# Kernel optimization log

Hardware: AMD Instinct MI355X
Metric: run time of the kernel (lower is better)

The kernel has to match this reference:

```python
import jax, jax.numpy as jnp
import numpy as np

B, T, H, I, O, R = 64, 1024, 1024, 8, 8, 4
NOISE_STD, ALPHA = 0.05, 0.2


def setup_inputs() -> dict:
    key = jax.random.key(0)
    ks = jax.random.split(key, 6)
    return {
        "x": jax.random.normal(ks[0], (B, T, I), jnp.float32),
        "noise": jax.random.normal(ks[1], (B, T, H), jnp.float32),
        "wi": jax.random.normal(ks[2], (I, H), jnp.float32),
        "si": jnp.ones((I,), jnp.float32),
        "m": jax.random.normal(ks[3], (H, R), jnp.float32),
        "n": jax.random.normal(ks[4], (H, R), jnp.float32),
        "b": jnp.zeros((H,), jnp.float32),
        "wo": jax.random.normal(ks[5], (H, O), jnp.float32) / H,
        "so": jnp.ones((O,), jnp.float32),
        "h0": jnp.zeros((H,), jnp.float32),
    }


def reference(x, noise, wi, si, m, n, b, wo, so, h0):
    hidden = h0.shape[0]
    batch = x.shape[0]
    wi_full = wi * si[:, None]          # (I, H): (wi.T * si).T
    wo_full = wo * so                   # (H, O)
    h_init = jnp.broadcast_to(h0, (batch, hidden))
    r_init = jnp.tanh(h_init)           # non_linearity(initial_states)
    # precompute input drive for all steps: (B,T,H) -> scan over time-major
    u = jnp.einsum('bti,ih->tbh', x, wi_full)
    noise_t = jnp.transpose(noise, (1, 0, 2))  # (T,B,H)

    def step(carry, inp):
        h, r = carry
        u_i, nz_i = inp
        rec = (r @ n) @ m.T / hidden                    # low-rank recurrence
        h = h + NOISE_STD * nz_i + ALPHA * (-h + rec + u_i)
        r = jnp.tanh(h + b)
        out = h @ wo_full                               # identity output nonlin
        return (h, r), out

    _, outs = jax.lax.scan(step, (h_init, r_init), (u, noise_t))
    return jnp.transpose(outs, (1, 0, 2))  # (B,T,O)
```

## Files before the change

### kernel.cpp

```cpp
#include <hip/hip_runtime.h>

#define BB 64
#define TT 1024
#define HH 1024
#define II 8
#define OO 8
#define RRK 4
#define NOISE_STD 0.05f
#define ALPHA 0.2f

typedef float v4f __attribute__((ext_vector_type(4)));

#define C2E 2.885390081777927f

template<int CTRL, int RM>
__device__ __forceinline__ float dpp_add(float acc, float src) {
    int s = __builtin_amdgcn_update_dpp(0, __float_as_int(src), CTRL, RM, 0xF, true);
    return acc + __int_as_float(s);
}

__device__ __forceinline__ float wave_sum(float x) {
    x = dpp_add<0xB1, 0xF>(x, x);
    x = dpp_add<0x4E, 0xF>(x, x);
    x = dpp_add<0x141, 0xF>(x, x);
    x = dpp_add<0x140, 0xF>(x, x);
    x = dpp_add<0x142, 0xA>(x, x);
    x = dpp_add<0x143, 0xC>(x, x);
    return x;
}

__device__ __forceinline__ float tanh_from_l2x(float l2x) {
    float e = __builtin_amdgcn_exp2f(l2x);
    float r = __builtin_amdgcn_rcpf(e + 1.0f);
    return fmaf(-2.0f, r, 1.0f);
}

__device__ __forceinline__ void block_sync_lds() {
    asm volatile("s_waitcnt lgkmcnt(0)\n\ts_barrier" ::: "memory");
}


__global__ __launch_bounds__(256)
void pre_d_kernel(const float* __restrict__ x, const float* __restrict__ noise,
                  const float* __restrict__ wi, const float* __restrict__ si,
                  const float* __restrict__ wo, const float* __restrict__ so,
                  float* __restrict__ d, float* __restrict__ sbase) {
    __shared__ __align__(16) float red[2][8][4][8];

    const int tid  = threadIdx.x;
    const int wave = tid >> 6;
    const int lane = tid & 63;
    const int e0   = tid << 2;

    v4f wia4[II];
    #pragma unroll
    for (int i = 0; i < II; ++i)
        wia4[i] = (ALPHA * si[i]) * *(const v4f*)(wi + (size_t)i * HH + e0);

    float woa[4][OO];
    #pragma unroll
    for (int e = 0; e < 4; ++e) {
        const float4 a4 = *(const float4*)(wo + (e0 + e) * OO);
        const float4 b4 = *(const float4*)(wo + (e0 + e) * OO + 4);
        woa[e][0] = a4.x * so[0]; woa[e][1] = a4.y * so[1];
        woa[e][2] = a4.z * so[2]; woa[e][3] = a4.w * so[3];
        woa[e][4] = b4.x * so[4]; woa[e][5] = b4.y * so[5];
        woa[e][6] = b4.z * so[6]; woa[e][7] = b4.w * so[7];
    }

    const int row0 = blockIdx.x * 32;
    float4 nz[8], nzn[8];
    #pragma unroll
    for (int j = 0; j < 8; ++j)
        nz[j] = *(const float4*)(noise + (size_t)(row0 + j) * HH + e0);

    #pragma unroll
    for (int ph = 0; ph < 4; ++ph) {
        const int cur   = ph & 1;
        const int rbase = row0 + ph * 8;

        if (ph < 3) {
            #pragma unroll
            for (int j = 0; j < 8; ++j)
                nzn[j] = *(const float4*)(noise + (size_t)(rbase + 8 + j) * HH + e0);
        }

        #pragma unroll
        for (int j = 0; j < 8; ++j) {
            const int row = rbase + j;
            const float4 xr0 = *(const float4*)(x + (size_t)row * II);
            const float4 xr1 = *(const float4*)(x + (size_t)row * II + 4);
            v4f u = xr0.x * wia4[0];
            u += xr0.y * wia4[1];  u += xr0.z * wia4[2];
            u += xr0.w * wia4[3];  u += xr1.x * wia4[4];
            u += xr1.y * wia4[5];  u += xr1.z * wia4[6];
            u += xr1.w * wia4[7];
            v4f d4 = u;
            d4.x = fmaf(NOISE_STD, nz[j].x, d4.x);
            d4.y = fmaf(NOISE_STD, nz[j].y, d4.y);
            d4.z = fmaf(NOISE_STD, nz[j].z, d4.z);
            d4.w = fmaf(NOISE_STD, nz[j].w, d4.w);
            *(v4f*)(d + (size_t)row * HH + e0) = d4;

            float op[OO];
            #pragma unroll
            for (int o = 0; o < OO; ++o)
                op[o] = fmaf(d4.x, woa[0][o], fmaf(d4.y, woa[1][o],
                        fmaf(d4.z, woa[2][o], d4.w * woa[3][o])));
            #pragma unroll
            for (int o = 0; o < OO; ++o) op[o] = wave_sum(op[o]);
            if (lane == 63) {
                *(float4*)&red[cur][j][wave][0] = make_float4(op[0], op[1], op[2], op[3]);
                *(float4*)&red[cur][j][wave][4] = make_float4(op[4], op[5], op[6], op[7]);
            }
        }
        block_sync_lds();
        if (tid < 64) {
            const int j = tid >> 3, o = tid & 7;
            sbase[(rbase + j) * OO + o] = (red[cur][j][0][o] + red[cur][j][1][o]) +
                                          (red[cur][j][2][o] + red[cur][j][3][o]);
        }
        #pragma unroll
        for (int j = 0; j < 8; ++j) nz[j] = nzn[j];
    }
}

__global__ __launch_bounds__(512, 1)
void rnn_pair(const float* __restrict__ d, const float* __restrict__ sbase,
              const float* __restrict__ mM, const float* __restrict__ nM,
              const float* __restrict__ bv, const float* __restrict__ wo,
              const float* __restrict__ so, const float* __restrict__ h0,
              float* __restrict__ out) {
    __shared__ __align__(16) float lds_v[2][TT * RRK];
    __shared__ __align__(16) float red[2][4][4][RRK];
    __shared__ __align__(16) float redc[8][40];
    __shared__ __align__(16) float amy[40];
    __shared__ __align__(16) float chs[2][32][OO];

    const int tid  = threadIdx.x;
    const int wave = tid >> 6;
    const int lane = tid & 63;
    const int sg   = wave >> 2;
    const int rw   = wave & 3;
    const int tl   = tid & 255;
    const int b    = blockIdx.x * 2 + sg;
    const int hb   = rw * 256 + lane * 4;
    const int oc   = tid & 7;

    {
        const int e2 = tid << 1;
        const float cs = ALPHA / (float)HH;
        const v4f m0 = cs * *(const v4f*)(mM + (size_t)e2 * RRK);
        const v4f m1 = cs * *(const v4f*)(mM + (size_t)(e2 + 1) * RRK);
        float wp0[OO], wp1[OO];
        {
            const float4 a4 = *(const float4*)(wo + (size_t)e2 * OO);
            const float4 b4 = *(const float4*)(wo + (size_t)e2 * OO + 4);
            wp0[0] = a4.x * so[0]; wp0[1] = a4.y * so[1];
            wp0[2] = a4.z * so[2]; wp0[3] = a4.w * so[3];
            wp0[4] = b4.x * so[4]; wp0[5] = b4.y * so[5];
            wp0[6] = b4.z * so[6]; wp0[7] = b4.w * so[7];
            const float4 c4 = *(const float4*)(wo + (size_t)(e2 + 1) * OO);
            const float4 d4 = *(const float4*)(wo + (size_t)(e2 + 1) * OO + 4);
            wp1[0] = c4.x * so[0]; wp1[1] = c4.y * so[1];
            wp1[2] = c4.z * so[2]; wp1[3] = c4.w * so[3];
            wp1[4] = d4.x * so[4]; wp1[5] = d4.y * so[5];
            wp1[6] = d4.z * so[6]; wp1[7] = d4.w * so[7];
        }
        const float ha = h0[e2], hc = h0[e2 + 1];
        #pragma unroll
        for (int kg = 0; kg < 10; ++kg) {
            float p[4];
            #pragma unroll
            for (int u = 0; u < 4; ++u) {
                const int k = kg * 4 + u;
                float s;
                if (k < 32) {
                    const int q = k >> 3, o = k & 7;
                    s = fmaf(m0[q], wp0[o], m1[q] * wp1[o]);
                } else {
                    const int o = k - 32;
                    s = fmaf(ha, wp0[o], hc * wp1[o]);
                }
                p[u] = wave_sum(s);
            }
            if (lane == 63)
                *(float4*)&redc[wave][kg * 4] = make_float4(p[0], p[1], p[2], p[3]);
        }
    }
    block_sync_lds();
    if (tid < 40)
        amy[tid] = ((redc[0][tid] + redc[1][tid]) + (redc[2][tid] + redc[3][tid])) +
                   ((redc[4][tid] + redc[5][tid]) + (redc[6][tid] + redc[7][tid]));

    v4f nrv[4], mac[RRK], h, r, tb2;
    {
        const float cs = ALPHA / (float)HH;
        v4f mrow[4];
        #pragma unroll
        for (int e = 0; e < 4; ++e) {
            nrv[e]  = *(const v4f*)(nM + (size_t)(hb + e) * RRK);
            mrow[e] = cs * *(const v4f*)(mM + (size_t)(hb + e) * RRK);
        }
        #pragma unroll
        for (int q = 0; q < RRK; ++q)
            mac[q] = (v4f){mrow[0][q], mrow[1][q], mrow[2][q], mrow[3][q]};
        h   = *(const v4f*)(h0 + hb);
        tb2 = C2E * *(const v4f*)(bv + hb);
        const v4f tg = C2E * h;
        r.x = tanh_from_l2x(tg.x); r.y = tanh_from_l2x(tg.y);
        r.z = tanh_from_l2x(tg.z); r.w = tanh_from_l2x(tg.w);
    }

    const float* dp = d + (size_t)b * (TT * HH) + hb;
    v4f dbuf[4];
    #pragma unroll
    for (int j = 0; j < 4; ++j)
        dbuf[j] = *(const v4f*)(dp + (size_t)j * HH);

    for (int t0 = 0; t0 < TT; t0 += 4) {
        #pragma unroll
        for (int j = 0; j < 4; ++j) {
            const int t = t0 + j;

            v4f vp = r.x * nrv[0];
            vp += r.y * nrv[1];
            vp += r.z * nrv[2];
            vp += r.w * nrv[3];
            const float s0 = wave_sum(vp.x);
            const float s1 = wave_sum(vp.y);
            const float s2 = wave_sum(vp.z);
            const float s3 = wave_sum(vp.w);
            if (lane == 63)
                *(float4*)&red[sg][j][rw][0] = make_float4(s0, s1, s2, s3);

            block_sync_lds();

            const v4f p0 = *(const v4f*)&red[sg][j][0][0];
            const v4f p1 = *(const v4f*)&red[sg][j][1][0];
            const v4f p2 = *(const v4f*)&red[sg][j][2][0];
            const v4f p3 = *(const v4f*)&red[sg][j][3][0];
            const v4f vs = (p0 + p1) + (p2 + p3);
            if (tl == 0) *(v4f*)&lds_v[sg][t * RRK] = vs;

            v4f acc = dbuf[j];
            acc += vs.x * mac[0];
            acc += vs.y * mac[1];
            acc += vs.z * mac[2];
            acc += vs.w * mac[3];
            h = (1.0f - ALPHA) * h + acc;

            dbuf[j] = *(const v4f*)(dp + (size_t)((t + 4) & (TT - 1)) * HH);

            const v4f tg = C2E * h + tb2;
            r.x = tanh_from_l2x(tg.x); r.y = tanh_from_l2x(tg.y);
            r.z = tanh_from_l2x(tg.z); r.w = tanh_from_l2x(tg.w);
        }
    }

    __syncthreads();

    float Amr[RRK];
    #pragma unroll
    for (int q = 0; q < RRK; ++q) Amr[q] = amy[q * 8 + oc];

    const int c  = tl >> 3;
    const int tc = c * 32;
    float a32;
    {
        float a = 1.0f - ALPHA;
        a = a * a; a = a * a; a = a * a; a = a * a; a = a * a;
        a32 = a;
    }
    const float* sb = sbase + (size_t)b * (TT * OO);

    auto step_s = [&](int t) -> float {
        const v4f vv = *(const v4f*)&lds_v[sg][t * RRK];
        float s = sb[t * OO + oc];
        s = fmaf(vv.x, Amr[0], s); s = fmaf(vv.y, Amr[1], s);
        s = fmaf(vv.z, Amr[2], s); s = fmaf(vv.w, Amr[3], s);
        return s;
    };

    float L = 0.0f;
    #pragma unroll 4
    for (int jt = 0; jt < 32; ++jt)
        L = fmaf(1.0f - ALPHA, L, step_s(tc + jt));
    chs[sg][c][oc] = L;
    block_sync_lds();
    if (tl < OO) {
        float Y = amy[32 + tl];
        #pragma unroll 4
        for (int c2 = 0; c2 < 32; ++c2) {
            const float Lc = chs[sg][c2][tl];
            chs[sg][c2][tl] = Y;
            Y = fmaf(a32, Y, Lc);
        }
    }
    block_sync_lds();
    float yv = chs[sg][c][oc];
    float* ob = out + (size_t)b * (TT * OO);
    #pragma unroll 4
    for (int jt = 0; jt < 32; ++jt) {
        const int t = tc + jt;
        yv = fmaf(1.0f - ALPHA, yv, step_s(t));
        ob[t * OO + oc] = yv;
    }
}


__global__ __launch_bounds__(256)
void prew_fb(const float* __restrict__ noise, const float* __restrict__ wo,
             const float* __restrict__ so, float* __restrict__ W) {
    __shared__ __align__(16) float red[2][8][4][8];

    const int tid  = threadIdx.x;
    const int wave = tid >> 6;
    const int lane = tid & 63;
    const int e0   = tid << 2;

    float woa[4][OO];
    {
        float so8[OO];
        #pragma unroll
        for (int o = 0; o < OO; ++o) so8[o] = so[o] * NOISE_STD;
        #pragma unroll
        for (int e = 0; e < 4; ++e) {
            const float4 a4 = *(const float4*)(wo + (e0 + e) * OO);
            const float4 b4 = *(const float4*)(wo + (e0 + e) * OO + 4);
            woa[e][0] = a4.x * so8[0]; woa[e][1] = a4.y * so8[1];
            woa[e][2] = a4.z * so8[2]; woa[e][3] = a4.w * so8[3];
            woa[e][4] = b4.x * so8[4]; woa[e][5] = b4.y * so8[5];
            woa[e][6] = b4.z * so8[6]; woa[e][7] = b4.w * so8[7];
        }
    }

    const int row0 = blockIdx.x * 32;
    float4 nz[8], nzn[8];
    #pragma unroll
    for (int j = 0; j < 8; ++j)
        nz[j] = *(const float4*)(noise + (size_t)(row0 + j) * HH + e0);

    #pragma unroll
    for (int ph = 0; ph < 4; ++ph) {
        const int cur   = ph & 1;
        const int rbase = row0 + ph * 8;
        if (ph < 3) {
            #pragma unroll
            for (int j = 0; j < 8; ++j)
                nzn[j] = *(const float4*)(noise + (size_t)(rbase + 8 + j) * HH + e0);
        }
        #pragma unroll
        for (int j = 0; j < 8; ++j) {
            float op[OO];
            #pragma unroll
            for (int o = 0; o < OO; ++o)
                op[o] = fmaf(nz[j].x, woa[0][o], fmaf(nz[j].y, woa[1][o],
                        fmaf(nz[j].z, woa[2][o], nz[j].w * woa[3][o])));
            #pragma unroll
            for (int o = 0; o < OO; ++o) op[o] = wave_sum(op[o]);
            if (lane == 63) {
                *(float4*)&red[cur][j][wave][0] = make_float4(op[0], op[1], op[2], op[3]);
                *(float4*)&red[cur][j][wave][4] = make_float4(op[4], op[5], op[6], op[7]);
            }
        }
        block_sync_lds();
        if (tid < 64) {
            const int j = tid >> 3, o = tid & 7;
            W[(rbase + j) * OO + o] = (red[cur][j][0][o] + red[cur][j][1][o]) +
                                      (red[cur][j][2][o] + red[cur][j][3][o]);
        }
        #pragma unroll
        for (int j = 0; j < 8; ++j) nz[j] = nzn[j];
    }
}

__global__ __launch_bounds__(256, 1)
void rnn_fb(const float* __restrict__ x, const float* __restrict__ noise,
            const float* __restrict__ wi, const float* __restrict__ si,
            const float* __restrict__ mM, const float* __restrict__ nM,
            const float* __restrict__ bv, const float* __restrict__ wo,
            const float* __restrict__ so, const float* __restrict__ h0,
            const float* __restrict__ W, float* __restrict__ out) {
    __shared__ __align__(16) float lds_x[(TT + 1) * II];
    __shared__ __align__(16) float lds_W[TT * OO];
    __shared__ __align__(16) float lds_out[TT * OO];
    __shared__ __align__(16) float red[4][4][4];
    __shared__ __align__(16) float redc[4][104];
    __shared__ float ambx[104];

    const int tid  = threadIdx.x;
    const int b    = blockIdx.x;
    const int wave = tid >> 6;
    const int lane = tid & 63;
    const int e0   = tid << 2;
    const int oc   = tid & 7;

    {
        const float4* sx = (const float4*)(x + (size_t)b * (TT * II));
        const float4* sw = (const float4*)(W + (size_t)b * (TT * OO));
        float4* dx = (float4*)lds_x;
        float4* dw = (float4*)lds_W;
        #pragma unroll
        for (int k = 0; k < 8; ++k) {
            dx[k * 256 + tid] = sx[k * 256 + tid];
            dw[k * 256 + tid] = sw[k * 256 + tid];
        }
        if (tid < 2) dx[2048 + tid] = sx[2046 + tid];
    }

    float wia[II][4];
    v4f   wiac[II];
    #pragma unroll
    for (int i = 0; i < II; ++i) {
        const float s  = ALPHA * si[i];
        const float4 w = *(const float4*)(wi + i * HH + e0);
        wia[i][0] = w.x * s; wia[i][1] = w.y * s; wia[i][2] = w.z * s; wia[i][3] = w.w * s;
        wiac[i] = (v4f){wia[i][0], wia[i][1], wia[i][2], wia[i][3]};
    }
    float ma[4][RRK];
    v4f   nrv[4];
    v4f   mac[RRK];
    #pragma unroll
    for (int e = 0; e < 4; ++e) {
        const float4 m4 = *(const float4*)(mM + (e0 + e) * RRK);
        const float4 n4 = *(const float4*)(nM + (e0 + e) * RRK);
        const float cs = ALPHA / (float)HH;
        ma[e][0] = m4.x * cs; ma[e][1] = m4.y * cs; ma[e][2] = m4.z * cs; ma[e][3] = m4.w * cs;
        nrv[e] = (v4f){n4.x, n4.y, n4.z, n4.w};
    }
    #pragma unroll
    for (int q = 0; q < RRK; ++q)
        mac[q] = (v4f){ma[0][q], ma[1][q], ma[2][q], ma[3][q]};

    float woa[4][OO];
    {
        #pragma unroll
        for (int e = 0; e < 4; ++e) {
            const float4 a4 = *(const float4*)(wo + (e0 + e) * OO);
            const float4 b4 = *(const float4*)(wo + (e0 + e) * OO + 4);
            woa[e][0] = a4.x * so[0]; woa[e][1] = a4.y * so[1];
            woa[e][2] = a4.z * so[2]; woa[e][3] = a4.w * so[3];
            woa[e][4] = b4.x * so[4]; woa[e][5] = b4.y * so[5];
            woa[e][6] = b4.z * so[6]; woa[e][7] = b4.w * so[7];
        }
    }
    v4f tb2e, h, rr;
    {
        const v4f b4 = *(const v4f*)(bv + e0);
        tb2e = C2E * b4;
        h = *(const v4f*)(h0 + e0);
        v4f targ = C2E * h;
        rr.x = tanh_from_l2x(targ.x); rr.y = tanh_from_l2x(targ.y);
        rr.z = tanh_from_l2x(targ.z); rr.w = tanh_from_l2x(targ.w);
    }

    #pragma unroll
    for (int kg = 0; kg < 26; ++kg) {
        float p[4];
        #pragma unroll
        for (int u = 0; u < 4; ++u) {
            const int k = kg * 4 + u;
            float s;
            if (k < 32) {
                const int q = k >> 3, o = k & 7;
                s = fmaf(ma[0][q], woa[0][o], fmaf(ma[1][q], woa[1][o],
                    fmaf(ma[2][q], woa[2][o], ma[3][q] * woa[3][o])));
            } else if (k < 96) {
                const int i = (k - 32) >> 3, o = k & 7;
                s = fmaf(wia[i][0], woa[0][o], fmaf(wia[i][1], woa[1][o],
                    fmaf(wia[i][2], woa[2][o], wia[i][3] * woa[3][o])));
            } else {
                const int o = k - 96;
                s = fmaf(h.x, woa[0][o], fmaf(h.y, woa[1][o],
                    fmaf(h.z, woa[2][o], h.w * woa[3][o])));
            }
            p[u] = wave_sum(s);
        }
        if (lane == 63)
            *(float4*)&redc[wave][kg * 4] = make_float4(p[0], p[1], p[2], p[3]);
    }
    block_sync_lds();
    if (tid < 104)
        ambx[tid] = (redc[0][tid] + redc[1][tid]) + (redc[2][tid] + redc[3][tid]);
    __syncthreads();

    float Amr[RRK], Bxr[II], y;
    #pragma unroll
    for (int q = 0; q < RRK; ++q) Amr[q] = ambx[q * 8 + oc];
    #pragma unroll
    for (int i = 0; i < II; ++i) Bxr[i] = ambx[32 + i * 8 + oc];
    y = ambx[96 + oc];

    const float* nzp = noise + (size_t)b * (TT * HH) + e0;
    v4f nzb[4];
    #pragma unroll
    for (int j = 0; j < 4; ++j) nzb[j] = *(const v4f*)(nzp + j * HH);

    v4f xqc0 = *(const v4f*)&lds_x[0];
    v4f xqc1 = *(const v4f*)&lds_x[4];
    float wqc = lds_W[oc];

    for (int t0 = 0; t0 < TT; t0 += 4) {
        #pragma unroll
        for (int j = 0; j < 4; ++j) {
            const int t = t0 + j;
            const int tn = t + 1;
            const v4f xqn0 = *(const v4f*)&lds_x[tn * II];
            const v4f xqn1 = *(const v4f*)&lds_x[tn * II + 4];
            const float wqn = lds_W[(tn & (TT - 1)) * OO + oc];

            v4f vpv = rr.x * nrv[0];
            vpv += rr.y * nrv[1];
            vpv += rr.z * nrv[2];
            vpv += rr.w * nrv[3];
            float vp0 = wave_sum(vpv.x);
            float vp1 = wave_sum(vpv.y);
            float vp2 = wave_sum(vpv.z);
            float vp3 = wave_sum(vpv.w);
            if (lane == 63)
                *(float4*)&red[j][wave][0] = make_float4(vp0, vp1, vp2, vp3);

            float ybase = fmaf(xqc0.x, Bxr[0], wqc);
            ybase = fmaf(xqc0.y, Bxr[1], ybase);
            ybase = fmaf(xqc0.z, Bxr[2], ybase);
            ybase = fmaf(xqc0.w, Bxr[3], ybase);
            ybase = fmaf(xqc1.x, Bxr[4], ybase);
            ybase = fmaf(xqc1.y, Bxr[5], ybase);
            ybase = fmaf(xqc1.z, Bxr[6], ybase);
            ybase = fmaf(xqc1.w, Bxr[7], ybase);

            v4f auv = xqc0.x * wiac[0];
            auv += xqc0.y * wiac[1];
            auv += xqc0.z * wiac[2];
            auv += xqc0.w * wiac[3];
            auv += xqc1.x * wiac[4];
            auv += xqc1.y * wiac[5];
            auv += xqc1.z * wiac[6];
            auv += xqc1.w * wiac[7];

            block_sync_lds();

            const v4f s0 = *(const v4f*)&red[j][0][0];
            const v4f s1 = *(const v4f*)&red[j][1][0];
            const v4f s2 = *(const v4f*)&red[j][2][0];
            const v4f s3 = *(const v4f*)&red[j][3][0];
            const v4f vs = (s0 + s1) + (s2 + s3);

            v4f acc = auv;
            acc += vs.x * mac[0];
            acc += vs.y * mac[1];
            acc += vs.z * mac[2];
            acc += vs.w * mac[3];
            h = (1.0f - ALPHA) * h + acc;
            h += NOISE_STD * nzb[j];

            {
                float t4 = fmaf(vs.x, Amr[0], ybase);
                t4 = fmaf(vs.y, Amr[1], t4);
                t4 = fmaf(vs.z, Amr[2], t4);
                t4 = fmaf(vs.w, Amr[3], t4);
                y = fmaf(1.0f - ALPHA, y, t4);
                if (tid < OO) lds_out[t * OO + tid] = y;
            }

            nzb[j] = *(const v4f*)(nzp + ((t + 4) & (TT - 1)) * HH);

            {
                v4f targ = C2E * h + tb2e;
                rr.x = tanh_from_l2x(targ.x);
                rr.y = tanh_from_l2x(targ.y);
                rr.z = tanh_from_l2x(targ.z);
                rr.w = tanh_from_l2x(targ.w);
            }
            xqc0 = xqn0; xqc1 = xqn1; wqc = wqn;
        }
    }

    __syncthreads();
    {
        float4* dst = (float4*)(out + (size_t)b * (TT * OO));
        const float4* srcv = (const float4*)lds_out;
        #pragma unroll
        for (int k = 0; k < 8; ++k)
            dst[k * 256 + tid] = srcv[k * 256 + tid];
    }
}

extern "C" void kernel_launch(void* const* d_in, const int* in_sizes, int n_in,
                              void* d_out, int out_size, void* d_ws, size_t ws_size,
                              hipStream_t stream) {
    const float* x     = (const float*)d_in[0];
    const float* noise = (const float*)d_in[1];
    const float* wi    = (const float*)d_in[2];
    const float* si    = (const float*)d_in[3];
    const float* mM    = (const float*)d_in[4];
    const float* nM    = (const float*)d_in[5];
    const float* bv    = (const float*)d_in[6];
    const float* wo    = (const float*)d_in[7];
    const float* so    = (const float*)d_in[8];
    const float* h0    = (const float*)d_in[9];
    float* out = (float*)d_out;

    const size_t needD = (size_t)BB * TT * HH * sizeof(float);
    const size_t needS = (size_t)BB * TT * OO * sizeof(float);

    if (ws_size >= needD + needS) {
        float* dbuf = (float*)d_ws;
        float* sb   = dbuf + (size_t)BB * TT * HH;
        pre_d_kernel<<<dim3(2048), dim3(256), 0, stream>>>(
            x, noise, wi, si, wo, so, dbuf, sb);
        rnn_pair<<<dim3(BB / 2), dim3(512), 0, stream>>>(
            dbuf, sb, mM, nM, bv, wo, so, h0, out);
    } else {
        float* W = (float*)d_ws;
        prew_fb<<<dim3(2048), dim3(256), 0, stream>>>(noise, wo, so, W);
        rnn_fb<<<dim3(BB), dim3(256), 0, stream>>>(
            x, noise, wi, si, mM, nM, bv, wo, so, h0, W, out);
    }
}
```

Baseline: 909.6 us.

## Interleave two batch recurrences per 256-thread block instead of two 256-thread subgroups

The recurrent kernel now uses 256 threads per block. Each thread carries the hidden state for both batch elements of the pair, so the two independent recurrences are interleaved inside one instruction stream and share one barrier per step. Before, each batch had its own 4-wave subgroup in a 512-thread block. The aim is to hide the latency of the serial reduction and tanh chain with independent work and to halve the waves that take part in each barrier. The cost is more registers and longer per-wave work per step, and the output scan now uses 64-step chunks.

```diff
diff --git a/kernel.cpp b/kernel.cpp
--- a/kernel.cpp
+++ b/kernel.cpp
@@ -33,6 +33,13 @@
     float e = __builtin_amdgcn_exp2f(l2x);
     float r = __builtin_amdgcn_rcpf(e + 1.0f);
     return fmaf(-2.0f, r, 1.0f);
+}
+
+__device__ __forceinline__ v4f tanh4(v4f tg) {
+    v4f r;
+    r.x = tanh_from_l2x(tg.x); r.y = tanh_from_l2x(tg.y);
+    r.z = tanh_from_l2x(tg.z); r.w = tanh_from_l2x(tg.w);
+    return r;
 }
 
 __device__ __forceinline__ void block_sync_lds() {
@@ -125,78 +132,28 @@
     }
 }
 
-__global__ __launch_bounds__(512, 1)
-void rnn_pair(const float* __restrict__ d, const float* __restrict__ sbase,
-              const float* __restrict__ mM, const float* __restrict__ nM,
-              const float* __restrict__ bv, const float* __restrict__ wo,
-              const float* __restrict__ so, const float* __restrict__ h0,
-              float* __restrict__ out) {
+__global__ __launch_bounds__(256, 1)
+void rnn_pair2(const float* __restrict__ d, const float* __restrict__ sbase,
+               const float* __restrict__ mM, const float* __restrict__ nM,
+               const float* __restrict__ bv, const float* __restrict__ wo,
+               const float* __restrict__ so, const float* __restrict__ h0,
+               float* __restrict__ out) {
     __shared__ __align__(16) float lds_v[2][TT * RRK];
     __shared__ __align__(16) float red[2][4][4][RRK];
-    __shared__ __align__(16) float redc[8][40];
+    __shared__ __align__(16) float redc[4][40];
     __shared__ __align__(16) float amy[40];
-    __shared__ __align__(16) float chs[2][32][OO];
+    __shared__ __align__(16) float chs[2][16][OO];
 
     const int tid  = threadIdx.x;
     const int wave = tid >> 6;
     const int lane = tid & 63;
-    const int sg   = wave >> 2;
-    const int rw   = wave & 3;
-    const int tl   = tid & 255;
-    const int b    = blockIdx.x * 2 + sg;
-    const int hb   = rw * 256 + lane * 4;
+    const int hb   = tid << 2;
     const int oc   = tid & 7;
-
-    {
-        const int e2 = tid << 1;
+    const int bA   = blockIdx.x * 2;
+
+    v4f nrv[4], mrow[4], mac[RRK], tb2;
+    {
         const float cs = ALPHA / (float)HH;
-        const v4f m0 = cs * *(const v4f*)(mM + (size_t)e2 * RRK);
-        const v4f m1 = cs * *(const v4f*)(mM + (size_t)(e2 + 1) * RRK);
-        float wp0[OO], wp1[OO];
-        {
-            const float4 a4 = *(const float4*)(wo + (size_t)e2 * OO);
-            const float4 b4 = *(const float4*)(wo + (size_t)e2 * OO + 4);
-            wp0[0] = a4.x * so[0]; wp0[1] = a4.y * so[1];
-            wp0[2] = a4.z * so[2]; wp0[3] = a4.w * so[3];
-            wp0[4] = b4.x * so[4]; wp0[5] = b4.y * so[5];
-            wp0[6] = b4.z * so[6]; wp0[7] = b4.w * so[7];
-            const float4 c4 = *(const float4*)(wo + (size_t)(e2 + 1) * OO);
-            const float4 d4 = *(const float4*)(wo + (size_t)(e2 + 1) * OO + 4);
-            wp1[0] = c4.x * so[0]; wp1[1] = c4.y * so[1];
-            wp1[2] = c4.z * so[2]; wp1[3] = c4.w * so[3];
-            wp1[4] = d4.x * so[4]; wp1[5] = d4.y * so[5];
-            wp1[6] = d4.z * so[6]; wp1[7] = d4.w * so[7];
-        }
-        const float ha = h0[e2], hc = h0[e2 + 1];
-        #pragma unroll
-        for (int kg = 0; kg < 10; ++kg) {
-            float p[4];
-            #pragma unroll
-            for (int u = 0; u < 4; ++u) {
-                const int k = kg * 4 + u;
-                float s;
-                if (k < 32) {
-                    const int q = k >> 3, o = k & 7;
-                    s = fmaf(m0[q], wp0[o], m1[q] * wp1[o]);
-                } else {
-                    const int o = k - 32;
-                    s = fmaf(ha, wp0[o], hc * wp1[o]);
-                }
-                p[u] = wave_sum(s);
-            }
-            if (lane == 63)
-                *(float4*)&redc[wave][kg * 4] = make_float4(p[0], p[1], p[2], p[3]);
-        }
-    }
-    block_sync_lds();
-    if (tid < 40)
-        amy[tid] = ((redc[0][tid] + redc[1][tid]) + (redc[2][tid] + redc[3][tid])) +
-                   ((redc[4][tid] + redc[5][tid]) + (redc[6][tid] + redc[7][tid]));
-
-    v4f nrv[4], mac[RRK], h, r, tb2;
-    {
-        const float cs = ALPHA / (float)HH;
-        v4f mrow[4];
         #pragma unroll
         for (int e = 0; e < 4; ++e) {
             nrv[e]  = *(const v4f*)(nM + (size_t)(hb + e) * RRK);
@@ -205,56 +162,116 @@
         #pragma unroll
         for (int q = 0; q < RRK; ++q)
             mac[q] = (v4f){mrow[0][q], mrow[1][q], mrow[2][q], mrow[3][q]};
-        h   = *(const v4f*)(h0 + hb);
         tb2 = C2E * *(const v4f*)(bv + hb);
-        const v4f tg = C2E * h;
-        r.x = tanh_from_l2x(tg.x); r.y = tanh_from_l2x(tg.y);
-        r.z = tanh_from_l2x(tg.z); r.w = tanh_from_l2x(tg.w);
-    }
-
-    const float* dp = d + (size_t)b * (TT * HH) + hb;
-    v4f dbuf[4];
-    #pragma unroll
-    for (int j = 0; j < 4; ++j)
-        dbuf[j] = *(const v4f*)(dp + (size_t)j * HH);
+    }
+    v4f hA, hB, rA, rB, h0v;
+    {
+        h0v = *(const v4f*)(h0 + hb);
+        hA = h0v; hB = h0v;
+        rA = tanh4(C2E * h0v);
+        rB = rA;
+    }
+
+    {
+        float acc[40];
+        #pragma unroll
+        for (int k = 0; k < 40; ++k) acc[k] = 0.0f;
+        #pragma unroll
+        for (int e = 0; e < 4; ++e) {
+            const float4 a4 = *(const float4*)(wo + (size_t)(hb + e) * OO);
+            const float4 b4 = *(const float4*)(wo + (size_t)(hb + e) * OO + 4);
+            float wp[OO];
+            wp[0] = a4.x * so[0]; wp[1] = a4.y * so[1];
+            wp[2] = a4.z * so[2]; wp[3] = a4.w * so[3];
+            wp[4] = b4.x * so[4]; wp[5] = b4.y * so[5];
+            wp[6] = b4.z * so[6]; wp[7] = b4.w * so[7];
+            #pragma unroll
+            for (int q = 0; q < RRK; ++q) {
+                const float ms = mrow[e][q];
+                #pragma unroll
+                for (int o = 0; o < OO; ++o)
+                    acc[q * 8 + o] = fmaf(ms, wp[o], acc[q * 8 + o]);
+            }
+            const float hs = h0v[e];
+            #pragma unroll
+            for (int o = 0; o < OO; ++o)
+                acc[32 + o] = fmaf(hs, wp[o], acc[32 + o]);
+        }
+        #pragma unroll
+        for (int k = 0; k < 40; ++k) acc[k] = wave_sum(acc[k]);
+        if (lane == 63) {
+            #pragma unroll
+            for (int k = 0; k < 10; ++k)
+                *(float4*)&redc[wave][k * 4] = make_float4(acc[k*4+0], acc[k*4+1],
+                                                           acc[k*4+2], acc[k*4+3]);
+        }
+    }
+    block_sync_lds();
+    if (tid < 40)
+        amy[tid] = (redc[0][tid] + redc[1][tid]) + (redc[2][tid] + redc[3][tid]);
+    block_sync_lds();
+
+    const float* dpA = d + (size_t)bA * (TT * HH) + hb;
+    const float* dpB = dpA + (size_t)TT * HH;
+    v4f dbA[4], dbB[4];
+    #pragma unroll
+    for (int j = 0; j < 4; ++j) {
+        dbA[j] = *(const v4f*)(dpA + (size_t)j * HH);
+        dbB[j] = *(const v4f*)(dpB + (size_t)j * HH);
+    }
 
     for (int t0 = 0; t0 < TT; t0 += 4) {
         #pragma unroll
         for (int j = 0; j < 4; ++j) {
             const int t = t0 + j;
 
-            v4f vp = r.x * nrv[0];
-            vp += r.y * nrv[1];
-            vp += r.z * nrv[2];
-            vp += r.w * nrv[3];
-            const float s0 = wave_sum(vp.x);
-            const float s1 = wave_sum(vp.y);
-            const float s2 = wave_sum(vp.z);
-            const float s3 = wave_sum(vp.w);
-            if (lane == 63)
-                *(float4*)&red[sg][j][rw][0] = make_float4(s0, s1, s2, s3);
+            {
+                v4f vp = rA.x * nrv[0];
+                vp += rA.y * nrv[1]; vp += rA.z * nrv[2]; vp += rA.w * nrv[3];
+                const float s0 = wave_sum(vp.x); const float s1 = wave_sum(vp.y);
+                const float s2 = wave_sum(vp.z); const float s3 = wave_sum(vp.w);
+                if (lane == 63)
+                    *(float4*)&red[0][j][wave][0] = make_float4(s0, s1, s2, s3);
+            }
+            {
+                v4f vp = rB.x * nrv[0];
+                vp += rB.y * nrv[1]; vp += rB.z * nrv[2]; vp += rB.w * nrv[3];
+                const float s0 = wave_sum(vp.x); const float s1 = wave_sum(vp.y);
+                const float s2 = wave_sum(vp.z); const float s3 = wave_sum(vp.w);
+                if (lane == 63)
+                    *(float4*)&red[1][j][wave][0] = make_float4(s0, s1, s2, s3);
+            }
 
             block_sync_lds();
 
-            const v4f p0 = *(const v4f*)&red[sg][j][0][0];
-            const v4f p1 = *(const v4f*)&red[sg][j][1][0];
-            const v4f p2 = *(const v4f*)&red[sg][j][2][0];
-            const v4f p3 = *(const v4f*)&red[sg][j][3][0];
-            const v4f vs = (p0 + p1) + (p2 + p3);
-            if (tl == 0) *(v4f*)&lds_v[sg][t * RRK] = vs;
-
-            v4f acc = dbuf[j];
-            acc += vs.x * mac[0];
-            acc += vs.y * mac[1];
-            acc += vs.z * mac[2];
-            acc += vs.w * mac[3];
-            h = (1.0f - ALPHA) * h + acc;
-
-            dbuf[j] = *(const v4f*)(dp + (size_t)((t + 4) & (TT - 1)) * HH);
-
-            const v4f tg = C2E * h + tb2;
-            r.x = tanh_from_l2x(tg.x); r.y = tanh_from_l2x(tg.y);
-            r.z = tanh_from_l2x(tg.z); r.w = tanh_from_l2x(tg.w);
+            {
+                const v4f p0 = *(const v4f*)&red[0][j][0][0];
+                const v4f p1 = *(const v4f*)&red[0][j][1][0];
+                const v4f p2 = *(const v4f*)&red[0][j][2][0];
+                const v4f p3 = *(const v4f*)&red[0][j][3][0];
+                const v4f vs = (p0 + p1) + (p2 + p3);
+                if (tid == 0) *(v4f*)&lds_v[0][t * RRK] = vs;
+                v4f acc = dbA[j];
+                acc += vs.x * mac[0]; acc += vs.y * mac[1];
+                acc += vs.z * mac[2]; acc += vs.w * mac[3];
+                hA = (1.0f - ALPHA) * hA + acc;
+                dbA[j] = *(const v4f*)(dpA + (size_t)((t + 4) & (TT - 1)) * HH);
+                rA = tanh4(C2E * hA + tb2);
+            }
+            {
+                const v4f p0 = *(const v4f*)&red[1][j][0][0];
+                const v4f p1 = *(const v4f*)&red[1][j][1][0];
+                const v4f p2 = *(const v4f*)&red[1][j][2][0];
+                const v4f p3 = *(const v4f*)&red[1][j][3][0];
+                const v4f vs = (p0 + p1) + (p2 + p3);
+                if (tid == 64) *(v4f*)&lds_v[1][t * RRK] = vs;
+                v4f acc = dbB[j];
+                acc += vs.x * mac[0]; acc += vs.y * mac[1];
+                acc += vs.z * mac[2]; acc += vs.w * mac[3];
+                hB = (1.0f - ALPHA) * hB + acc;
+                dbB[j] = *(const v4f*)(dpB + (size_t)((t + 4) & (TT - 1)) * HH);
+                rB = tanh4(C2E * hB + tb2);
+            }
         }
     }
 
@@ -264,15 +281,18 @@
     #pragma unroll
     for (int q = 0; q < RRK; ++q) Amr[q] = amy[q * 8 + oc];
 
-    const int c  = tl >> 3;
-    const int tc = c * 32;
-    float a32;
+    const int cg = tid >> 3;
+    const int sg = cg >> 4;
+    const int cc = cg & 15;
+    const int tc = cc * 64;
+    float a64;
     {
         float a = 1.0f - ALPHA;
-        a = a * a; a = a * a; a = a * a; a = a * a; a = a * a;
-        a32 = a;
-    }
-    const float* sb = sbase + (size_t)b * (TT * OO);
+        #pragma unroll
+        for (int k = 0; k < 6; ++k) a = a * a;
+        a64 = a;
+    }
+    const float* sb = sbase + (size_t)(bA + sg) * (TT * OO);
 
     auto step_s = [&](int t) -> float {
         const v4f vv = *(const v4f*)&lds_v[sg][t * RRK];
@@ -284,24 +304,25 @@
 
     float L = 0.0f;
     #pragma unroll 4
-    for (int jt = 0; jt < 32; ++jt)
+    for (int jt = 0; jt < 64; ++jt)
         L = fmaf(1.0f - ALPHA, L, step_s(tc + jt));
-    chs[sg][c][oc] = L;
+    chs[sg][cc][oc] = L;
     block_sync_lds();
-    if (tl < OO) {
-        float Y = amy[32 + tl];
-        #pragma unroll 4
-        for (int c2 = 0; c2 < 32; ++c2) {
-            const float Lc = chs[sg][c2][tl];
-            chs[sg][c2][tl] = Y;
-            Y = fmaf(a32, Y, Lc);
+    if (tid < 16) {
+        const int s2 = tid >> 3, o = tid & 7;
+        float Y = amy[32 + o];
+        #pragma unroll
+        for (int c2 = 0; c2 < 16; ++c2) {
+            const float Lc = chs[s2][c2][o];
+            chs[s2][c2][o] = Y;
+            Y = fmaf(a64, Y, Lc);
         }
     }
     block_sync_lds();
-    float yv = chs[sg][c][oc];
-    float* ob = out + (size_t)b * (TT * OO);
+    float yv = chs[sg][cc][oc];
+    float* ob = out + (size_t)(bA + sg) * (TT * OO);
     #pragma unroll 4
-    for (int jt = 0; jt < 32; ++jt) {
+    for (int jt = 0; jt < 64; ++jt) {
         const int t = tc + jt;
         yv = fmaf(1.0f - ALPHA, yv, step_s(t));
         ob[t * OO + oc] = yv;
@@ -610,7 +631,7 @@
         float* sb   = dbuf + (size_t)BB * TT * HH;
         pre_d_kernel<<<dim3(2048), dim3(256), 0, stream>>>(
             x, noise, wi, si, wo, so, dbuf, sb);
-        rnn_pair<<<dim3(BB / 2), dim3(512), 0, stream>>>(
+        rnn_pair2<<<dim3(BB / 2), dim3(256), 0, stream>>>(
             dbuf, sb, mM, nM, bv, wo, so, h0, out);
     } else {
         float* W = (float*)d_ws;
```

Measured after the change: 1.100 ms. 21.0% more time.
